# Kernel optimization log

Hardware: AMD Instinct MI355X
Metric: run time of the kernel (lower is better)

## Reference

```python
import jax, jax.numpy as jnp
import numpy as np

N_NODES = 100000
N_EDGES = 600000
IN_DIM = 128
HID = 128
OUT_DIM = 64
N_LAYERS = 3


def setup_inputs() -> dict:
    key = jax.random.key(0)
    ks = jax.random.split(key, 8)
    x = jax.random.normal(ks[0], (N_NODES, IN_DIM), dtype=jnp.float32)
    edge_index = jax.random.randint(ks[1], (2, N_EDGES), 0, N_NODES, dtype=jnp.int64)
    s = 1.0 / np.sqrt(HID)
    W_in = jax.random.normal(ks[2], (HID, IN_DIM), dtype=jnp.float32) * s
    b_in = jax.random.normal(ks[3], (HID,), dtype=jnp.float32) * s
    W_convs = jax.random.normal(ks[4], (N_LAYERS, HID, HID), dtype=jnp.float32) * s
    b_convs = jax.random.normal(ks[5], (N_LAYERS, HID), dtype=jnp.float32) * s
    W_out = jax.random.normal(ks[6], (OUT_DIM, (N_LAYERS + 1) * HID), dtype=jnp.float32) * s
    b_out = jax.random.normal(ks[7], (OUT_DIM,), dtype=jnp.float32) * s
    return {"x": x, "edge_index": edge_index, "W_in": W_in, "b_in": b_in,
            "W_convs": W_convs, "b_convs": b_convs, "W_out": W_out, "b_out": b_out}


def reference(x, edge_index, W_in, b_in, W_convs, b_convs, W_out, b_out):
    src, dst = edge_index[0], edge_index[1]
    n = x.shape[0]
    # input projection: [N, in] -> [N, H]
    h = x @ W_in.T + b_in
    hidden_states = [h]
    for i in range(W_convs.shape[0]):
        # GINConv (eps=0): nn(x + sum of neighbor messages), messages src->dst
        agg = jax.ops.segment_sum(h[src], dst, num_segments=n)
        h = (h + agg) @ W_convs[i].T + b_convs[i]
        hidden_states.append(h)
    cat = jnp.concatenate(hidden_states, axis=1)  # [N, (L+1)*H]
    out = cat @ W_out.T + b_out  # [N, OUT]
    return jax.nn.softmax(out, axis=-1)
```

## Files before the change

kernel.cpp:

```cpp
#include <hip/hip_runtime.h>
#include <hip/hip_bf16.h>
#include <hip/hip_fp16.h>

#define GN 100000
#define GE 600000
#define SCAN_NBLK 98
#define ALD 132

typedef __bf16    bf16x8 __attribute__((ext_vector_type(8)));
typedef _Float16  f16x8  __attribute__((ext_vector_type(8)));
typedef float     f32x4  __attribute__((ext_vector_type(4)));

__global__ __launch_bounds__(256) void convert_w(
    const float* __restrict__ Win, const float* __restrict__ Wc,
    const float* __restrict__ Wout,
    __bf16* __restrict__ hi, __bf16* __restrict__ lo)
{
    const int i = blockIdx.x * 256 + threadIdx.x;
    if (i >= 98304) return;
    float v;
    if (i < 16384)      v = Win[i];
    else if (i < 65536) v = Wc[i - 16384];
    else                v = Wout[i - 65536];
    const __bf16 h = (__bf16)v;
    hi[i] = h;
    lo[i] = (__bf16)(v - (float)h);
}

__global__ __launch_bounds__(256, 8) void gather_rows(
    const uint* __restrict__ Hw,
    const int* __restrict__ row_start,
    const int* __restrict__ deg,
    const int* __restrict__ csr,
    float* __restrict__ Aggp)
{
    const int wave = threadIdx.x >> 6;
    const int lane = threadIdx.x & 63;
    const int row  = blockIdx.x * 4 + wave;
    if (row >= GN) return;

    const uint self = Hw[(size_t)row * 64 + lane];
    const int start = row_start[row];
    const int dg    = deg[row];
    float2 acc = make_float2(0.f, 0.f);

    for (int b = 0; b < dg; b += 64) {
        const int n = min(dg - b, 64);
        const int idx = csr[start + min(b + lane, dg - 1)];
        for (int k = 0; k < n; k += 8) {
            uint t[8];
#pragma unroll
            for (int u = 0; u < 8; ++u) {
                const int s = __shfl(idx, min(k + u, n - 1));
                t[u] = Hw[(size_t)s * 64 + lane];
            }
            const int m = min(n - k, 8);
#pragma unroll
            for (int u = 0; u < 8; ++u) {
                if (u < m) {
                    union { uint uu; _Float16 h[2]; } cv;
                    cv.uu = t[u];
                    acc.x += (float)cv.h[0];
                    acc.y += (float)cv.h[1];
                }
            }
        }
    }

    union { uint uu; _Float16 h[2]; } sv;
    sv.uu = self;
    acc.x += (float)sv.h[0];
    acc.y += (float)sv.h[1];

    *(float2*)&Aggp[(size_t)row * 128 + lane * 2] = acc;
}

__device__ __forceinline__ void gemm_tile(
    const float* __restrict__ AccBuf,
    const __bf16* __restrict__ Whi, const __bf16* __restrict__ Wlo,
    const int wn, const int quad, const int l15,
    f32x4 acc[2][2])
{
#pragma unroll
    for (int i = 0; i < 2; ++i)
#pragma unroll
        for (int j = 0; j < 2; ++j) acc[i][j] = (f32x4)(0.0f);

    bf16x8 whA[2], wlA[2], whB[2], wlB[2];
#pragma unroll
    for (int nt = 0; nt < 2; ++nt) {
        const int n = wn + nt * 16 + l15;
        whA[nt] = *(const bf16x8*)(Whi + (size_t)n * 128 + quad * 8);
        wlA[nt] = *(const bf16x8*)(Wlo + (size_t)n * 128 + quad * 8);
    }
#pragma unroll
    for (int ks = 0; ks < 4; ++ks) {
        const int kt = ks * 32 + quad * 8;
        if (ks < 3) {
            const int kn = kt + 32;
#pragma unroll
            for (int nt = 0; nt < 2; ++nt) {
                const int n = wn + nt * 16 + l15;
                whB[nt] = *(const bf16x8*)(Whi + (size_t)n * 128 + kn);
                wlB[nt] = *(const bf16x8*)(Wlo + (size_t)n * 128 + kn);
            }
        }
        bf16x8 ahi[2], alo[2];
#pragma unroll
        for (int mt = 0; mt < 2; ++mt) {
            const float* ap = &AccBuf[(mt * 16 + l15) * ALD + kt];
            const f32x4 p = *(const f32x4*)ap;
            const f32x4 q = *(const f32x4*)(ap + 4);
#pragma unroll
            for (int e = 0; e < 4; ++e) {
                const __bf16 hp = (__bf16)p[e];
                const __bf16 hq = (__bf16)q[e];
                ahi[mt][e]     = hp;
                ahi[mt][e + 4] = hq;
                alo[mt][e]     = (__bf16)(p[e] - (float)hp);
                alo[mt][e + 4] = (__bf16)(q[e] - (float)hq);
            }
        }
#pragma unroll
        for (int mt = 0; mt < 2; ++mt)
#pragma unroll
            for (int nt = 0; nt < 2; ++nt) {
                acc[mt][nt] = __builtin_amdgcn_mfma_f32_16x16x32_bf16(
                    ahi[mt], whA[nt], acc[mt][nt], 0, 0, 0);
                acc[mt][nt] = __builtin_amdgcn_mfma_f32_16x16x32_bf16(
                    ahi[mt], wlA[nt], acc[mt][nt], 0, 0, 0);
                acc[mt][nt] = __builtin_amdgcn_mfma_f32_16x16x32_bf16(
                    alo[mt], whA[nt], acc[mt][nt], 0, 0, 0);
            }
        if (ks < 3) {
#pragma unroll
            for (int nt = 0; nt < 2; ++nt) {
                whA[nt] = whB[nt];
                wlA[nt] = wlB[nt];
            }
        }
    }
}

template<bool AGGIN>
__global__ __launch_bounds__(256, 3) void gin_layer(
    const float* __restrict__ Hf32,
    const __bf16* __restrict__ Whi,
    const __bf16* __restrict__ Wlo,
    const float* __restrict__ bias,
    _Float16* __restrict__ Hout)
{
    __shared__ float Acc[32 * ALD];

    const int tid  = threadIdx.x;
    const int wave = tid >> 6;
    const int lane = tid & 63;
    const int row0 = blockIdx.x * 32;
    const int wn   = wave * 32;
    const int quad = lane >> 4;
    const int l15  = lane & 15;
    const int c8   = l15 * 8;

#pragma unroll
    for (int p = 0; p < 2; ++p) {
        const int r = wave * 8 + p * 4 + quad;
        const size_t g = (size_t)(row0 + r) * 128 + c8;
        const f32x4 v0 = *(const f32x4*)(Hf32 + g);
        const f32x4 v1 = *(const f32x4*)(Hf32 + g + 4);
        *(f32x4*)&Acc[r * ALD + c8]     = v0;
        *(f32x4*)&Acc[r * ALD + c8 + 4] = v1;
    }
    __syncthreads();

    f32x4 acc[2][2];
    gemm_tile(Acc, Whi, Wlo, wn, quad, l15, acc);
    __syncthreads();

#pragma unroll
    for (int nt = 0; nt < 2; ++nt) {
        const int col = wn + nt * 16 + l15;
        const float b = bias[col];
#pragma unroll
        for (int mt = 0; mt < 2; ++mt)
#pragma unroll
            for (int r4 = 0; r4 < 4; ++r4)
                Acc[(mt * 16 + quad * 4 + r4) * ALD + col] = acc[mt][nt][r4] + b;
    }
    __syncthreads();
#pragma unroll
    for (int p = 0; p < 2; ++p) {
        const int q = tid + p * 256;
        const int r = q >> 4;
        const int g = (q & 15) * 8;
        const float4 a = *(const float4*)&Acc[r * ALD + g];
        const float4 b = *(const float4*)&Acc[r * ALD + g + 4];
        f16x8 o = {(_Float16)a.x, (_Float16)a.y, (_Float16)a.z, (_Float16)a.w,
                   (_Float16)b.x, (_Float16)b.y, (_Float16)b.z, (_Float16)b.w};
        *(f16x8*)&Hout[(size_t)(row0 + r) * 128 + g] = o;
    }
}

__global__ __launch_bounds__(256, 3) void gin_final(
    const _Float16* __restrict__ h0,
    const _Float16* __restrict__ h1,
    const _Float16* __restrict__ h2,
    const float* __restrict__ Aggp,
    const __bf16* __restrict__ Whi3,
    const __bf16* __restrict__ Wlo3,
    const float* __restrict__ b3,
    const __bf16* __restrict__ WhiO,
    const __bf16* __restrict__ WloO,
    const float* __restrict__ bO,
    float* __restrict__ out)
{
    constexpr int CLD = 68;

    __shared__ float Smem[32 * ALD];
    float* const Acc = Smem;
    float* const Cst = Smem;

    const int tid  = threadIdx.x;
    const int wave = tid >> 6;
    const int lane = tid & 63;
    const int row0 = blockIdx.x * 32;
    const int quad = lane >> 4;
    const int l15  = lane & 15;
    const int c8   = l15 * 8;

#pragma unroll
    for (int p = 0; p < 2; ++p) {
        const int r = wave * 8 + p * 4 + quad;
        const size_t g = (size_t)(row0 + r) * 128 + c8;
        const f32x4 v0 = *(const f32x4*)(Aggp + g);
        const f32x4 v1 = *(const f32x4*)(Aggp + g + 4);
        *(f32x4*)&Acc[r * ALD + c8]     = v0;
        *(f32x4*)&Acc[r * ALD + c8 + 4] = v1;
    }
    __syncthreads();

    const int wn = wave * 32;
    f32x4 acc1[2][2];
    gemm_tile(Acc, Whi3, Wlo3, wn, quad, l15, acc1);
    __syncthreads();

#pragma unroll
    for (int nt = 0; nt < 2; ++nt) {
        const int col = wn + nt * 16 + l15;
        const float b = b3[col];
#pragma unroll
        for (int mt = 0; mt < 2; ++mt)
#pragma unroll
            for (int r4 = 0; r4 < 4; ++r4)
                Acc[(mt * 16 + quad * 4 + r4) * ALD + col] = acc1[mt][nt][r4] + b;
    }
    __syncthreads();

    const int wk  = wave & 1;
    const int wn2 = (wave >> 1) * 32;
    f32x4 acc2[2][2];
#pragma unroll
    for (int i = 0; i < 2; ++i)
#pragma unroll
        for (int j = 0; j < 2; ++j) acc2[i][j] = (f32x4)(0.0f);

    f16x8 hA[2], hB[2];
    bf16x8 whA[2], wlA[2], whB[2], wlB[2];

    {
        const int kg = wk * 256 + quad * 8;
        const _Float16* hb = (kg < 128) ? h0 : (kg < 256) ? h1 : h2;
        const int kc = kg & 127;
#pragma unroll
        for (int mt = 0; mt < 2; ++mt) {
            const int row = mt * 16 + l15;
            hA[mt] = *(const f16x8*)(hb + (size_t)(row0 + row) * 128 + kc);
        }
#pragma unroll
        for (int nt = 0; nt < 2; ++nt) {
            const int n = wn2 + nt * 16 + l15;
            whA[nt] = *(const bf16x8*)(WhiO + (size_t)n * 512 + kg);
            wlA[nt] = *(const bf16x8*)(WloO + (size_t)n * 512 + kg);
        }
    }

#pragma unroll
    for (int ks = 0; ks < 8; ++ks) {
        const int kgC = wk * 256 + ks * 32 + quad * 8;
        if (ks < 7) {
            const int kgN = kgC + 32;
            if (kgN < 384) {
                const _Float16* hb = (kgN < 128) ? h0 : (kgN < 256) ? h1 : h2;
                const int kc = kgN & 127;
#pragma unroll
                for (int mt = 0; mt < 2; ++mt) {
                    const int row = mt * 16 + l15;
                    hB[mt] = *(const f16x8*)(hb + (size_t)(row0 + row) * 128 + kc);
                }
            }
#pragma unroll
            for (int nt = 0; nt < 2; ++nt) {
                const int n = wn2 + nt * 16 + l15;
                whB[nt] = *(const bf16x8*)(WhiO + (size_t)n * 512 + kgN);
                wlB[nt] = *(const bf16x8*)(WloO + (size_t)n * 512 + kgN);
            }
        }
        bf16x8 ahi[2], alo[2];
#pragma unroll
        for (int mt = 0; mt < 2; ++mt) {
            if (kgC < 384) {
#pragma unroll
                for (int e = 0; e < 8; ++e) {
                    const float v = (float)hA[mt][e];
                    const __bf16 hp = (__bf16)v;
                    ahi[mt][e] = hp;
                    alo[mt][e] = (__bf16)(v - (float)hp);
                }
            } else {
                const int row = mt * 16 + l15;
                const float* ap = &Acc[row * ALD + (kgC - 384)];
                const f32x4 p = *(const f32x4*)ap;
                const f32x4 q = *(const f32x4*)(ap + 4);
#pragma unroll
                for (int e = 0; e < 4; ++e) {
                    const __bf16 hp = (__bf16)p[e];
                    const __bf16 hq = (__bf16)q[e];
                    ahi[mt][e]     = hp;
                    ahi[mt][e + 4] = hq;
                    alo[mt][e]     = (__bf16)(p[e] - (float)hp);
                    alo[mt][e + 4] = (__bf16)(q[e] - (float)hq);
                }
            }
        }
#pragma unroll
        for (int mt = 0; mt < 2; ++mt)
#pragma unroll
            for (int nt = 0; nt < 2; ++nt) {
                acc2[mt][nt] = __builtin_amdgcn_mfma_f32_16x16x32_bf16(
                    ahi[mt], whA[nt], acc2[mt][nt], 0, 0, 0);
                acc2[mt][nt] = __builtin_amdgcn_mfma_f32_16x16x32_bf16(
                    ahi[mt], wlA[nt], acc2[mt][nt], 0, 0, 0);
                acc2[mt][nt] = __builtin_amdgcn_mfma_f32_16x16x32_bf16(
                    alo[mt], whA[nt], acc2[mt][nt], 0, 0, 0);
            }
        if (ks < 7) {
#pragma unroll
            for (int mt = 0; mt < 2; ++mt) hA[mt] = hB[mt];
#pragma unroll
            for (int nt = 0; nt < 2; ++nt) { whA[nt] = whB[nt]; wlA[nt] = wlB[nt]; }
        }
    }

    __syncthreads();

    if (wk == 1) {
#pragma unroll
        for (int nt = 0; nt < 2; ++nt)
#pragma unroll
            for (int mt = 0; mt < 2; ++mt)
#pragma unroll
                for (int r4 = 0; r4 < 4; ++r4)
                    Cst[(mt * 16 + quad * 4 + r4) * CLD + wn2 + nt * 16 + l15]
                        = acc2[mt][nt][r4];
    }
    __syncthreads();
    if (wk == 0) {
#pragma unroll
        for (int nt = 0; nt < 2; ++nt) {
            const int col = wn2 + nt * 16 + l15;
            const float b = bO[col];
#pragma unroll
            for (int mt = 0; mt < 2; ++mt)
#pragma unroll
                for (int r4 = 0; r4 < 4; ++r4) {
                    const int idx = (mt * 16 + quad * 4 + r4) * CLD + col;
                    Cst[idx] = Cst[idx] + acc2[mt][nt][r4] + b;
                }
        }
    }
    __syncthreads();

    for (int i = 0; i < 8; ++i) {
        const int r = wave * 8 + i;
        const float v = Cst[r * CLD + lane];
        float m = v;
#pragma unroll
        for (int off = 32; off > 0; off >>= 1) m = fmaxf(m, __shfl_xor(m, off));
        const float e = __expf(v - m);
        float s = e;
#pragma unroll
        for (int off = 32; off > 0; off >>= 1) s += __shfl_xor(s, off);
        out[(size_t)(row0 + r) * 64 + lane] = e / s;
    }
}

__global__ __launch_bounds__(256) void count_deg(const int* __restrict__ dst,
                                                 int* __restrict__ deg)
{
    const int e = blockIdx.x * 256 + threadIdx.x;
    if (e < GE) atomicAdd(&deg[dst[e]], 1);
}

__global__ __launch_bounds__(256) void scan_pass1(const int* __restrict__ deg,
                                                  int* __restrict__ excl,
                                                  int* __restrict__ blockSums)
{
    __shared__ int s[256];
    const int t = threadIdx.x;
    const int base = blockIdx.x * 1024 + t * 4;

    int4 v = make_int4(0, 0, 0, 0);
    if (base + 3 < GN) {
        v = *(const int4*)(deg + base);
    } else {
        if (base + 0 < GN) v.x = deg[base + 0];
        if (base + 1 < GN) v.y = deg[base + 1];
        if (base + 2 < GN) v.z = deg[base + 2];
        if (base + 3 < GN) v.w = deg[base + 3];
    }
    const int mysum = v.x + v.y + v.z + v.w;
    s[t] = mysum;
    __syncthreads();
    for (int off = 1; off < 256; off <<= 1) {
        const int val = (t >= off) ? s[t - off] : 0;
        __syncthreads();
        s[t] += val;
        __syncthreads();
    }
    int4 o;
    o.x = s[t] - mysum;
    o.y = o.x + v.x;
    o.z = o.y + v.y;
    o.w = o.z + v.z;
    if (base + 3 < GN) {
        *(int4*)(excl + base) = o;
    } else {
        if (base + 0 < GN) excl[base + 0] = o.x;
        if (base + 1 < GN) excl[base + 1] = o.y;
        if (base + 2 < GN) excl[base + 2] = o.z;
        if (base + 3 < GN) excl[base + 3] = o.w;
    }
    if (t == 255) blockSums[blockIdx.x] = s[255];
}

__global__ __launch_bounds__(128) void scan_pass2(const int* __restrict__ blockSums,
                                                  int* __restrict__ blockOffs, int n)
{
    __shared__ int s[128];
    const int t = threadIdx.x;
    const int v = (t < n) ? blockSums[t] : 0;
    s[t] = v;
    __syncthreads();
    for (int off = 1; off < 128; off <<= 1) {
        const int val = (t >= off) ? s[t - off] : 0;
        __syncthreads();
        s[t] += val;
        __syncthreads();
    }
    if (t < n) blockOffs[t] = s[t] - v;
}

__global__ __launch_bounds__(256) void scan_pass3(int* __restrict__ excl,
                                                  const int* __restrict__ blockOffs,
                                                  int* __restrict__ cursor)
{
    const int i = blockIdx.x * 256 + threadIdx.x;
    if (i >= GN) return;
    const int v = excl[i] + blockOffs[i >> 10];
    excl[i]   = v;
    cursor[i] = v;
}

__global__ __launch_bounds__(256) void fill_csr(const int* __restrict__ src,
                                                const int* __restrict__ dst,
                                                int* __restrict__ cursor,
                                                int* __restrict__ csr)
{
    const int e = blockIdx.x * 256 + threadIdx.x;
    if (e >= GE) return;
    const int pos = atomicAdd(&cursor[dst[e]], 1);
    csr[pos] = src[e];
}

extern "C" void kernel_launch(void* const* d_in, const int* in_sizes, int n_in,
                              void* d_out, int out_size, void* d_ws, size_t ws_size,
                              hipStream_t stream)
{
    const float* x       = (const float*)d_in[0];
    const int*   src     = (const int*)d_in[1];
    const int*   dst     = ((const int*)d_in[1]) + GE;
    const float* W_in    = (const float*)d_in[2];
    const float* b_in    = (const float*)d_in[3];
    const float* W_convs = (const float*)d_in[4];
    const float* b_convs = (const float*)d_in[5];
    const float* W_out   = (const float*)d_in[6];
    const float* b_out   = (const float*)d_in[7];
    float*       out     = (float*)d_out;

    _Float16* h0   = (_Float16*)d_ws;
    _Float16* h1   = h0 + (size_t)GN * 128;
    _Float16* h2   = h1 + (size_t)GN * 128;
    float*    Aggp = (float*)(h2 + (size_t)GN * 128);
    int*      deg       = (int*)(Aggp + (size_t)GN * 128);
    int*      row_start = deg + GN;
    int*      cursor    = row_start + GN;
    int*      blockSums = cursor + GN;
    int*      blockOffs = blockSums + 128;
    int*      csr       = blockOffs + 128;
    __bf16*   Whi       = (__bf16*)(csr + GE);
    __bf16*   Wlo       = Whi + 98304;

    const dim3 blk(256);
    const dim3 gblk(256);
    const int edge_blocks   = (GE + 255) / 256;
    const int node_blocks   = (GN + 255) / 256;
    const int layer_blocks  = GN / 32;
    const int gather_blocks = (GN + 3) / 4;

    hipMemsetAsync(deg, 0, GN * sizeof(int), stream);
    count_deg<<<edge_blocks, blk, 0, stream>>>(dst, deg);
    scan_pass1<<<SCAN_NBLK, blk, 0, stream>>>(deg, row_start, blockSums);
    scan_pass2<<<1, 128, 0, stream>>>(blockSums, blockOffs, SCAN_NBLK);
    scan_pass3<<<node_blocks, blk, 0, stream>>>(row_start, blockOffs, cursor);
    fill_csr<<<edge_blocks, blk, 0, stream>>>(src, dst, cursor, csr);

    convert_w<<<(98304 + 255) / 256, blk, 0, stream>>>(W_in, W_convs, W_out, Whi, Wlo);

    gin_layer<false><<<layer_blocks, gblk, 0, stream>>>(
        x, Whi, Wlo, b_in, h0);

    gather_rows<<<gather_blocks, gblk, 0, stream>>>(
        (const uint*)h0, row_start, deg, csr, Aggp);
    gin_layer<true><<<layer_blocks, gblk, 0, stream>>>(
        Aggp, Whi + 16384, Wlo + 16384, b_convs, h1);

    gather_rows<<<gather_blocks, gblk, 0, stream>>>(
        (const uint*)h1, row_start, deg, csr, Aggp);
    gin_layer<true><<<layer_blocks, gblk, 0, stream>>>(
        Aggp, Whi + 32768, Wlo + 32768, b_convs + 128, h2);

    gather_rows<<<gather_blocks, gblk, 0, stream>>>(
        (const uint*)h2, row_start, deg, csr, Aggp);
    gin_final<<<layer_blocks, gblk, 0, stream>>>(
        h0, h1, h2, Aggp, Whi + 49152, Wlo + 49152, b_convs + 256,
        Whi + 65536, Wlo + 65536, b_out, out);
}
```

Measured before the change: 466.2 us.

## Fold last GIN layer into output projection and gather 64-wide projected features

```diff
diff --git a/kernel.cpp b/kernel.cpp
--- a/kernel.cpp
+++ b/kernel.cpp
@@ -19,12 +19,48 @@
     const int i = blockIdx.x * 256 + threadIdx.x;
     if (i >= 98304) return;
     float v;
-    if (i < 16384)      v = Win[i];
-    else if (i < 65536) v = Wc[i - 16384];
-    else                v = Wout[i - 65536];
+    if (i < 16384) {
+        v = Win[i];
+    } else if (i < 49152) {
+        v = Wc[i - 16384];
+    } else {
+        const int j   = i - 49152;
+        const int l   = j >> 14;
+        const int r   = j & 16383;
+        const int row = r >> 7;
+        const int k   = r & 127;
+        v = (row < 64) ? Wout[row * 512 + l * 128 + k] : 0.f;
+    }
     const __bf16 h = (__bf16)v;
     hi[i] = h;
     lo[i] = (__bf16)(v - (float)h);
+}
+
+__global__ __launch_bounds__(256) void w3p_prep(
+    const float* __restrict__ Wc, const float* __restrict__ Wout,
+    const float* __restrict__ b3, const float* __restrict__ bOut,
+    __bf16* __restrict__ hi, __bf16* __restrict__ lo,
+    float* __restrict__ cvec)
+{
+    const int i = blockIdx.x * 256 + threadIdx.x;
+    const float* W3 = Wc + 32768;
+    if (i < 8192) {
+        const int o = i >> 7;
+        const int k = i & 127;
+        float s = 0.f;
+        for (int j = 0; j < 128; ++j)
+            s += Wout[o * 512 + 384 + j] * W3[j * 128 + k];
+        const __bf16 h = (__bf16)s;
+        const int idx = 81920 + (64 + o) * 128 + k;
+        hi[idx] = h;
+        lo[idx] = (__bf16)(s - (float)h);
+    }
+    if (blockIdx.x == 0 && threadIdx.x < 64) {
+        float c = bOut[threadIdx.x];
+        for (int j = 0; j < 128; ++j)
+            c += Wout[threadIdx.x * 512 + 384 + j] * b3[j];
+        cvec[threadIdx.x] = c;
+    }
 }
 
 __global__ __launch_bounds__(256, 8) void gather_rows(
@@ -75,6 +111,42 @@
     *(float2*)&Aggp[(size_t)row * 128 + lane * 2] = acc;
 }
 
+__global__ __launch_bounds__(256, 8) void gather_rows64(
+    const float* __restrict__ Y,
+    const int* __restrict__ row_start,
+    const int* __restrict__ deg,
+    const int* __restrict__ csr,
+    float* __restrict__ Aggy)
+{
+    const int wave = threadIdx.x >> 6;
+    const int lane = threadIdx.x & 63;
+    const int row  = blockIdx.x * 4 + wave;
+    if (row >= GN) return;
+
+    const float self = Y[(size_t)row * 64 + lane];
+    const int start = row_start[row];
+    const int dg    = deg[row];
+    float acc = 0.f;
+
+    for (int b = 0; b < dg; b += 64) {
+        const int n = min(dg - b, 64);
+        const int idx = csr[start + min(b + lane, dg - 1)];
+        for (int k = 0; k < n; k += 8) {
+            float t[8];
+#pragma unroll
+            for (int u = 0; u < 8; ++u) {
+                const int s = __shfl(idx, min(k + u, n - 1));
+                t[u] = Y[(size_t)s * 64 + lane];
+            }
+            const int m = min(n - k, 8);
+#pragma unroll
+            for (int u = 0; u < 8; ++u)
+                if (u < m) acc += t[u];
+        }
+    }
+    Aggy[(size_t)row * 64 + lane] = acc + self;
+}
+
 __device__ __forceinline__ void gemm_tile(
     const float* __restrict__ AccBuf,
     const __bf16* __restrict__ Whi, const __bf16* __restrict__ Wlo,
@@ -142,13 +214,17 @@
     }
 }
 
-template<bool AGGIN>
+template<int MODE>
 __global__ __launch_bounds__(256, 3) void gin_layer(
-    const float* __restrict__ Hf32,
+    const float* __restrict__ in,
     const __bf16* __restrict__ Whi,
     const __bf16* __restrict__ Wlo,
     const float* __restrict__ bias,
-    _Float16* __restrict__ Hout)
+    const __bf16* __restrict__ Ehi,
+    const __bf16* __restrict__ Elo,
+    _Float16* __restrict__ Hout,
+    float* __restrict__ partial,
+    float* __restrict__ y2)
 {
     __shared__ float Acc[32 * ALD];
 
@@ -165,15 +241,15 @@
     for (int p = 0; p < 2; ++p) {
         const int r = wave * 8 + p * 4 + quad;
         const size_t g = (size_t)(row0 + r) * 128 + c8;
-        const f32x4 v0 = *(const f32x4*)(Hf32 + g);
-        const f32x4 v1 = *(const f32x4*)(Hf32 + g + 4);
+        const f32x4 v0 = *(const f32x4*)(in + g);
+        const f32x4 v1 = *(const f32x4*)(in + g + 4);
         *(f32x4*)&Acc[r * ALD + c8]     = v0;
         *(f32x4*)&Acc[r * ALD + c8 + 4] = v1;
     }
     __syncthreads();
 
-    f32x4 acc[2][2];
-    gemm_tile(Acc, Whi, Wlo, wn, quad, l15, acc);
+    f32x4 acc1[2][2];
+    gemm_tile(Acc, Whi, Wlo, wn, quad, l15, acc1);
     __syncthreads();
 
 #pragma unroll
@@ -184,213 +260,84 @@
         for (int mt = 0; mt < 2; ++mt)
 #pragma unroll
             for (int r4 = 0; r4 < 4; ++r4)
-                Acc[(mt * 16 + quad * 4 + r4) * ALD + col] = acc[mt][nt][r4] + b;
-    }
-    __syncthreads();
-#pragma unroll
-    for (int p = 0; p < 2; ++p) {
-        const int q = tid + p * 256;
-        const int r = q >> 4;
-        const int g = (q & 15) * 8;
-        const float4 a = *(const float4*)&Acc[r * ALD + g];
-        const float4 b = *(const float4*)&Acc[r * ALD + g + 4];
-        f16x8 o = {(_Float16)a.x, (_Float16)a.y, (_Float16)a.z, (_Float16)a.w,
-                   (_Float16)b.x, (_Float16)b.y, (_Float16)b.z, (_Float16)b.w};
-        *(f16x8*)&Hout[(size_t)(row0 + r) * 128 + g] = o;
-    }
-}
-
-__global__ __launch_bounds__(256, 3) void gin_final(
-    const _Float16* __restrict__ h0,
-    const _Float16* __restrict__ h1,
-    const _Float16* __restrict__ h2,
-    const float* __restrict__ Aggp,
-    const __bf16* __restrict__ Whi3,
-    const __bf16* __restrict__ Wlo3,
-    const float* __restrict__ b3,
-    const __bf16* __restrict__ WhiO,
-    const __bf16* __restrict__ WloO,
-    const float* __restrict__ bO,
-    float* __restrict__ out)
-{
-    constexpr int CLD = 68;
-
-    __shared__ float Smem[32 * ALD];
-    float* const Acc = Smem;
-    float* const Cst = Smem;
-
-    const int tid  = threadIdx.x;
-    const int wave = tid >> 6;
-    const int lane = tid & 63;
-    const int row0 = blockIdx.x * 32;
-    const int quad = lane >> 4;
-    const int l15  = lane & 15;
-    const int c8   = l15 * 8;
-
-#pragma unroll
-    for (int p = 0; p < 2; ++p) {
-        const int r = wave * 8 + p * 4 + quad;
-        const size_t g = (size_t)(row0 + r) * 128 + c8;
-        const f32x4 v0 = *(const f32x4*)(Aggp + g);
-        const f32x4 v1 = *(const f32x4*)(Aggp + g + 4);
-        *(f32x4*)&Acc[r * ALD + c8]     = v0;
-        *(f32x4*)&Acc[r * ALD + c8 + 4] = v1;
-    }
-    __syncthreads();
-
-    const int wn = wave * 32;
-    f32x4 acc1[2][2];
-    gemm_tile(Acc, Whi3, Wlo3, wn, quad, l15, acc1);
+                Acc[(mt * 16 + quad * 4 + r4) * ALD + col] = acc1[mt][nt][r4] + b;
+    }
+    __syncthreads();
+
+    if (MODE < 2) {
+#pragma unroll
+        for (int p = 0; p < 2; ++p) {
+            const int q = tid + p * 256;
+            const int r = q >> 4;
+            const int g = (q & 15) * 8;
+            const float4 a = *(const float4*)&Acc[r * ALD + g];
+            const float4 b = *(const float4*)&Acc[r * ALD + g + 4];
+            f16x8 o = {(_Float16)a.x, (_Float16)a.y, (_Float16)a.z, (_Float16)a.w,
+                       (_Float16)b.x, (_Float16)b.y, (_Float16)b.z, (_Float16)b.w};
+            *(f16x8*)&Hout[(size_t)(row0 + r) * 128 + g] = o;
+        }
+    }
+
+    f32x4 acc2[2][2];
+    gemm_tile(Acc, Ehi, Elo, wn, quad, l15, acc2);
     __syncthreads();
 
 #pragma unroll
     for (int nt = 0; nt < 2; ++nt) {
         const int col = wn + nt * 16 + l15;
-        const float b = b3[col];
 #pragma unroll
         for (int mt = 0; mt < 2; ++mt)
 #pragma unroll
             for (int r4 = 0; r4 < 4; ++r4)
-                Acc[(mt * 16 + quad * 4 + r4) * ALD + col] = acc1[mt][nt][r4] + b;
-    }
-    __syncthreads();
-
-    const int wk  = wave & 1;
-    const int wn2 = (wave >> 1) * 32;
-    f32x4 acc2[2][2];
-#pragma unroll
-    for (int i = 0; i < 2; ++i)
-#pragma unroll
-        for (int j = 0; j < 2; ++j) acc2[i][j] = (f32x4)(0.0f);
-
-    f16x8 hA[2], hB[2];
-    bf16x8 whA[2], wlA[2], whB[2], wlB[2];
+                Acc[(mt * 16 + quad * 4 + r4) * ALD + col] = acc2[mt][nt][r4];
+    }
+    __syncthreads();
 
     {
-        const int kg = wk * 256 + quad * 8;
-        const _Float16* hb = (kg < 128) ? h0 : (kg < 256) ? h1 : h2;
-        const int kc = kg & 127;
-#pragma unroll
-        for (int mt = 0; mt < 2; ++mt) {
-            const int row = mt * 16 + l15;
-            hA[mt] = *(const f16x8*)(hb + (size_t)(row0 + row) * 128 + kc);
-        }
-#pragma unroll
-        for (int nt = 0; nt < 2; ++nt) {
-            const int n = wn2 + nt * 16 + l15;
-            whA[nt] = *(const bf16x8*)(WhiO + (size_t)n * 512 + kg);
-            wlA[nt] = *(const bf16x8*)(WloO + (size_t)n * 512 + kg);
-        }
-    }
-
-#pragma unroll
-    for (int ks = 0; ks < 8; ++ks) {
-        const int kgC = wk * 256 + ks * 32 + quad * 8;
-        if (ks < 7) {
-            const int kgN = kgC + 32;
-            if (kgN < 384) {
-                const _Float16* hb = (kgN < 128) ? h0 : (kgN < 256) ? h1 : h2;
-                const int kc = kgN & 127;
-#pragma unroll
-                for (int mt = 0; mt < 2; ++mt) {
-                    const int row = mt * 16 + l15;
-                    hB[mt] = *(const f16x8*)(hb + (size_t)(row0 + row) * 128 + kc);
-                }
-            }
-#pragma unroll
-            for (int nt = 0; nt < 2; ++nt) {
-                const int n = wn2 + nt * 16 + l15;
-                whB[nt] = *(const bf16x8*)(WhiO + (size_t)n * 512 + kgN);
-                wlB[nt] = *(const bf16x8*)(WloO + (size_t)n * 512 + kgN);
-            }
-        }
-        bf16x8 ahi[2], alo[2];
-#pragma unroll
-        for (int mt = 0; mt < 2; ++mt) {
-            if (kgC < 384) {
-#pragma unroll
-                for (int e = 0; e < 8; ++e) {
-                    const float v = (float)hA[mt][e];
-                    const __bf16 hp = (__bf16)v;
-                    ahi[mt][e] = hp;
-                    alo[mt][e] = (__bf16)(v - (float)hp);
-                }
-            } else {
-                const int row = mt * 16 + l15;
-                const float* ap = &Acc[row * ALD + (kgC - 384)];
-                const f32x4 p = *(const f32x4*)ap;
-                const f32x4 q = *(const f32x4*)(ap + 4);
-#pragma unroll
-                for (int e = 0; e < 4; ++e) {
-                    const __bf16 hp = (__bf16)p[e];
-                    const __bf16 hq = (__bf16)q[e];
-                    ahi[mt][e]     = hp;
-                    ahi[mt][e + 4] = hq;
-                    alo[mt][e]     = (__bf16)(p[e] - (float)hp);
-                    alo[mt][e + 4] = (__bf16)(q[e] - (float)hq);
-                }
-            }
-        }
-#pragma unroll
-        for (int mt = 0; mt < 2; ++mt)
-#pragma unroll
-            for (int nt = 0; nt < 2; ++nt) {
-                acc2[mt][nt] = __builtin_amdgcn_mfma_f32_16x16x32_bf16(
-                    ahi[mt], whA[nt], acc2[mt][nt], 0, 0, 0);
-                acc2[mt][nt] = __builtin_amdgcn_mfma_f32_16x16x32_bf16(
-                    ahi[mt], wlA[nt], acc2[mt][nt], 0, 0, 0);
-                acc2[mt][nt] = __builtin_amdgcn_mfma_f32_16x16x32_bf16(
-                    alo[mt], whA[nt], acc2[mt][nt], 0, 0, 0);
-            }
-        if (ks < 7) {
-#pragma unroll
-            for (int mt = 0; mt < 2; ++mt) hA[mt] = hB[mt];
-#pragma unroll
-            for (int nt = 0; nt < 2; ++nt) { whA[nt] = whB[nt]; wlA[nt] = wlB[nt]; }
-        }
-    }
-
-    __syncthreads();
-
-    if (wk == 1) {
-#pragma unroll
-        for (int nt = 0; nt < 2; ++nt)
-#pragma unroll
-            for (int mt = 0; mt < 2; ++mt)
-#pragma unroll
-                for (int r4 = 0; r4 < 4; ++r4)
-                    Cst[(mt * 16 + quad * 4 + r4) * CLD + wn2 + nt * 16 + l15]
-                        = acc2[mt][nt][r4];
-    }
-    __syncthreads();
-    if (wk == 0) {
-#pragma unroll
-        for (int nt = 0; nt < 2; ++nt) {
-            const int col = wn2 + nt * 16 + l15;
-            const float b = bO[col];
-#pragma unroll
-            for (int mt = 0; mt < 2; ++mt)
-#pragma unroll
-                for (int r4 = 0; r4 < 4; ++r4) {
-                    const int idx = (mt * 16 + quad * 4 + r4) * CLD + col;
-                    Cst[idx] = Cst[idx] + acc2[mt][nt][r4] + b;
-                }
-        }
-    }
-    __syncthreads();
-
-    for (int i = 0; i < 8; ++i) {
-        const int r = wave * 8 + i;
-        const float v = Cst[r * CLD + lane];
-        float m = v;
-#pragma unroll
-        for (int off = 32; off > 0; off >>= 1) m = fmaxf(m, __shfl_xor(m, off));
-        const float e = __expf(v - m);
-        float s = e;
-#pragma unroll
-        for (int off = 32; off > 0; off >>= 1) s += __shfl_xor(s, off);
-        out[(size_t)(row0 + r) * 64 + lane] = e / s;
-    }
+        const int r  = tid >> 3;
+        const int cc = (tid & 7) * 8;
+        const size_t gp = (size_t)(row0 + r) * 64 + cc;
+        f32x4 z0 = *(const f32x4*)&Acc[r * ALD + cc];
+        f32x4 z1 = *(const f32x4*)&Acc[r * ALD + cc + 4];
+        if (MODE == 0) {
+            *(f32x4*)&partial[gp]     = z0;
+            *(f32x4*)&partial[gp + 4] = z1;
+        } else {
+            const f32x4 p0 = *(const f32x4*)&partial[gp];
+            const f32x4 p1 = *(const f32x4*)&partial[gp + 4];
+            *(f32x4*)&partial[gp]     = p0 + z0;
+            *(f32x4*)&partial[gp + 4] = p1 + z1;
+        }
+        if (MODE == 2) {
+            const f32x4 w0 = *(const f32x4*)&Acc[r * ALD + 64 + cc];
+            const f32x4 w1 = *(const f32x4*)&Acc[r * ALD + 64 + cc + 4];
+            *(f32x4*)&y2[gp]     = w0;
+            *(f32x4*)&y2[gp + 4] = w1;
+        }
+    }
+}
+
+__global__ __launch_bounds__(256, 8) void final_softmax(
+    const float* __restrict__ pre,
+    const float* __restrict__ aggy,
+    const float* __restrict__ cvec,
+    float* __restrict__ out)
+{
+    const int wave = threadIdx.x >> 6;
+    const int lane = threadIdx.x & 63;
+    const int row  = blockIdx.x * 4 + wave;
+    if (row >= GN) return;
+
+    const size_t g = (size_t)row * 64 + lane;
+    const float v = pre[g] + aggy[g] + cvec[lane];
+    float m = v;
+#pragma unroll
+    for (int off = 32; off > 0; off >>= 1) m = fmaxf(m, __shfl_xor(m, off));
+    const float e = __expf(v - m);
+    float s = e;
+#pragma unroll
+    for (int off = 32; off > 0; off >>= 1) s += __shfl_xor(s, off);
+    out[g] = e / s;
 }
 
 __global__ __launch_bounds__(256) void count_deg(const int* __restrict__ dst,
@@ -496,11 +443,14 @@
     const float* b_out   = (const float*)d_in[7];
     float*       out     = (float*)d_out;
 
-    _Float16* h0   = (_Float16*)d_ws;
-    _Float16* h1   = h0 + (size_t)GN * 128;
-    _Float16* h2   = h1 + (size_t)GN * 128;
-    float*    Aggp = (float*)(h2 + (size_t)GN * 128);
-    int*      deg       = (int*)(Aggp + (size_t)GN * 128);
+    _Float16* h0      = (_Float16*)d_ws;
+    _Float16* h1      = h0 + (size_t)GN * 128;
+    float*    Aggp    = (float*)(h1 + (size_t)GN * 128);
+    float*    partial = Aggp + (size_t)GN * 128;
+    float*    y2      = partial + (size_t)GN * 64;
+    float*    Aggy    = y2 + (size_t)GN * 64;
+    float*    cvec    = Aggy + (size_t)GN * 64;
+    int*      deg       = (int*)(cvec + 128);
     int*      row_start = deg + GN;
     int*      cursor    = row_start + GN;
     int*      blockSums = cursor + GN;
@@ -524,23 +474,25 @@
     fill_csr<<<edge_blocks, blk, 0, stream>>>(src, dst, cursor, csr);
 
     convert_w<<<(98304 + 255) / 256, blk, 0, stream>>>(W_in, W_convs, W_out, Whi, Wlo);
-
-    gin_layer<false><<<layer_blocks, gblk, 0, stream>>>(
-        x, Whi, Wlo, b_in, h0);
+    w3p_prep<<<32, blk, 0, stream>>>(W_convs, W_out, b_convs + 256, b_out,
+                                     Whi, Wlo, cvec);
+
+    gin_layer<0><<<layer_blocks, gblk, 0, stream>>>(
+        x, Whi, Wlo, b_in, Whi + 49152, Wlo + 49152, h0, partial, nullptr);
 
     gather_rows<<<gather_blocks, gblk, 0, stream>>>(
         (const uint*)h0, row_start, deg, csr, Aggp);
-    gin_layer<true><<<layer_blocks, gblk, 0, stream>>>(
-        Aggp, Whi + 16384, Wlo + 16384, b_convs, h1);
+    gin_layer<1><<<layer_blocks, gblk, 0, stream>>>(
+        Aggp, Whi + 16384, Wlo + 16384, b_convs,
+        Whi + 65536, Wlo + 65536, h1, partial, nullptr);
 
     gather_rows<<<gather_blocks, gblk, 0, stream>>>(
         (const uint*)h1, row_start, deg, csr, Aggp);
-    gin_layer<true><<<layer_blocks, gblk, 0, stream>>>(
-        Aggp, Whi + 32768, Wlo + 32768, b_convs + 128, h2);
-
-    gather_rows<<<gather_blocks, gblk, 0, stream>>>(
-        (const uint*)h2, row_start, deg, csr, Aggp);
-    gin_final<<<layer_blocks, gblk, 0, stream>>>(
-        h0, h1, h2, Aggp, Whi + 49152, Wlo + 49152, b_convs + 256,
-        Whi + 65536, Wlo + 65536, b_out, out);
-}
+    gin_layer<2><<<layer_blocks, gblk, 0, stream>>>(
+        Aggp, Whi + 32768, Wlo + 32768, b_convs + 128,
+        Whi + 81920, Wlo + 81920, nullptr, partial, y2);
+
+    gather_rows64<<<gather_blocks, gblk, 0, stream>>>(
+        y2, row_start, deg, csr, Aggy);
+    final_softmax<<<gather_blocks, gblk, 0, stream>>>(partial, Aggy, cvec, out);
+}
```

Measured after the change: 475.1 us. Within noise of the previous version (+1.9%).
